# Performance work log

Hardware: AMD Instinct MI355X
Metric: run time of the kernel (lower is better)

## Reference

```python
import jax, jax.numpy as jnp
import numpy as np

B, S, D, H = 8, 1024, 768, 12
DH = D // H
EPS = 1e-5


def setup_inputs() -> dict:
    key = jax.random.key(0)
    ks = jax.random.split(key, 12)
    sc_h = 1.0 / np.sqrt(DH)
    sc_d = 1.0 / np.sqrt(D)
    return {
        "x": jax.random.normal(ks[0], (B, S, D), jnp.float32),
        "ln1_g": jnp.ones((D,), jnp.float32),
        "ln1_b": jnp.zeros((D,), jnp.float32),
        "Wq": jax.random.normal(ks[1], (H, DH, DH), jnp.float32) * sc_h,
        "bq": jax.random.normal(ks[2], (H, DH), jnp.float32) * 0.01,
        "Wk": jax.random.normal(ks[3], (H, DH, DH), jnp.float32) * sc_h,
        "bk": jax.random.normal(ks[4], (H, DH), jnp.float32) * 0.01,
        "Wv": jax.random.normal(ks[5], (H, DH, DH), jnp.float32) * sc_h,
        "bv": jax.random.normal(ks[6], (H, DH), jnp.float32) * 0.01,
        "ln2_g": jnp.ones((D,), jnp.float32),
        "ln2_b": jnp.zeros((D,), jnp.float32),
        "W1": jax.random.normal(ks[7], (D, 4 * D), jnp.float32) * sc_d,  # c_fc (bias=False)
        "W2": jax.random.normal(ks[8], (4 * D, D), jnp.float32) * (1.0 / np.sqrt(4 * D)),  # c_proj (bias=False)
    }


def _layernorm(x, g, b):
    m = jnp.mean(x, axis=-1, keepdims=True)
    v = jnp.mean(jnp.square(x - m), axis=-1, keepdims=True)
    return (x - m) * jax.lax.rsqrt(v + EPS) * g + b


def _msa(x, Wq, bq, Wk, bk, Wv, bv):
    b, s, d = x.shape
    h = x.reshape(b, s, H, DH)  # per-head slices of the embedding
    q = jnp.einsum('bshd,hde->bhse', h, Wq) + bq[None, :, None, :]
    k = jnp.einsum('bshd,hde->bhse', h, Wk) + bk[None, :, None, :]
    v = jnp.einsum('bshd,hde->bhse', h, Wv) + bv[None, :, None, :]
    scores = jnp.einsum('bhse,bhte->bhst', q, k) / np.sqrt(DH).astype(np.float32)
    attn = jax.nn.softmax(scores, axis=-1)
    o = jnp.einsum('bhst,bhte->bhse', attn, v)
    return o.transpose(0, 2, 1, 3).reshape(b, s, d)  # concat heads


def reference(x, ln1_g, ln1_b, Wq, bq, Wk, bk, Wv, bv, ln2_g, ln2_b, W1, W2):
    out = x + _msa(_layernorm(x, ln1_g, ln1_b), Wq, bq, Wk, bk, Wv, bv)
    h = _layernorm(out, ln2_g, ln2_b)
    ffn = jnp.dot(jax.nn.gelu(jnp.dot(h, W1), approximate=False), W2)
    return out + ffn
```

## Files before the change

kernel.cpp:

```cpp
#include <hip/hip_runtime.h>
#include <hip/hip_bf16.h>
#include <math.h>

#define B_ 8
#define S_ 1024
#define D_ 768
#define H_ 12
#define QSCALE 0.18033688011112042f

typedef __attribute__((ext_vector_type(8))) short short8;
typedef __attribute__((ext_vector_type(4))) float floatx4;
typedef unsigned short ushort_t;

__device__ __forceinline__ ushort_t f2bf(float f) {
  unsigned int u = __builtin_bit_cast(unsigned int, f);
  u += 0x7fffu + ((u >> 16) & 1u);
  return (ushort_t)(u >> 16);
}

__device__ __forceinline__ unsigned int pkbf(float a, float b) {
  __hip_bfloat162 h = __float22bfloat162_rn(make_float2(a, b));
  unsigned int r;
  __builtin_memcpy(&r, &h, sizeof(r));
  return r;
}

__device__ __forceinline__ float gelu_f(float x) {
  const float z = fabsf(x) * 0.70710678118654752f;
  const float t = __builtin_amdgcn_rcpf(1.0f + 0.3275911f * z);
  const float p =
      t * (0.254829592f +
           t * (-0.284496736f +
                t * (1.421413741f + t * (-1.453152027f + t * 1.061405429f))));
  const float e = __expf(-z * z);
  const float erfv = 1.0f - p * e;
  return 0.5f * x * (1.0f + copysignf(erfv, x));
}

template <int N>
__device__ __forceinline__ void wait_vmcnt() {
  if constexpr (N == 0)
    asm volatile("s_waitcnt vmcnt(0)" ::: "memory");
  else if constexpr (N == 3)
    asm volatile("s_waitcnt vmcnt(3)" ::: "memory");
  else if constexpr (N == 4)
    asm volatile("s_waitcnt vmcnt(4)" ::: "memory");
  else if constexpr (N == 6)
    asm volatile("s_waitcnt vmcnt(6)" ::: "memory");
  else
    asm volatile("s_waitcnt vmcnt(8)" ::: "memory");
}

__global__ __launch_bounds__(256) void ln_bf16(
    const float* __restrict__ in, const float* __restrict__ g,
    const float* __restrict__ bias, ushort_t* __restrict__ out) {
  const int row = blockIdx.x * 4 + (threadIdx.x >> 6);
  const int lane = threadIdx.x & 63;
  const float* p = in + (size_t)row * D_;
  float4 v[3];
#pragma unroll
  for (int j = 0; j < 3; ++j) v[j] = *(const float4*)(p + j * 256 + lane * 4);
  float s = 0.f;
#pragma unroll
  for (int j = 0; j < 3; ++j) s += (v[j].x + v[j].y) + (v[j].z + v[j].w);
#pragma unroll
  for (int m = 1; m < 64; m <<= 1) s += __shfl_xor(s, m);
  const float mean = s * (1.0f / D_);
  float q = 0.f;
#pragma unroll
  for (int j = 0; j < 3; ++j) {
    const float a = v[j].x - mean, b = v[j].y - mean;
    const float c = v[j].z - mean, d = v[j].w - mean;
    q += (a * a + b * b) + (c * c + d * d);
  }
#pragma unroll
  for (int m = 1; m < 64; m <<= 1) q += __shfl_xor(q, m);
  const float rstd = rsqrtf(q * (1.0f / D_) + 1e-5f);
  ushort_t* o = out + (size_t)row * D_;
#pragma unroll
  for (int j = 0; j < 3; ++j) {
    const float4 gv = *(const float4*)(g + j * 256 + lane * 4);
    const float4 bv = *(const float4*)(bias + j * 256 + lane * 4);
    const unsigned int p01 = pkbf((v[j].x - mean) * rstd * gv.x + bv.x,
                                  (v[j].y - mean) * rstd * gv.y + bv.y);
    const unsigned int p23 = pkbf((v[j].z - mean) * rstd * gv.z + bv.z,
                                  (v[j].w - mean) * rstd * gv.w + bv.w);
    *(uint2*)(o + j * 256 + lane * 4) = make_uint2(p01, p23);
  }
}

__global__ __launch_bounds__(256) void transpose_cast(
    const float* __restrict__ W, ushort_t* __restrict__ Wt, int Kdim, int Ndim) {
  __shared__ float tile[32][33];
  const int n0 = blockIdx.x * 32, k0 = blockIdx.y * 32;
  const int tx = threadIdx.x & 31, ty = threadIdx.x >> 5;
#pragma unroll
  for (int i = 0; i < 32; i += 8)
    tile[ty + i][tx] = W[(size_t)(k0 + ty + i) * Ndim + n0 + tx];
  __syncthreads();
#pragma unroll
  for (int i = 0; i < 32; i += 8)
    Wt[(size_t)(n0 + ty + i) * Kdim + k0 + tx] = f2bf(tile[tx][ty + i]);
}

__global__ __launch_bounds__(256) void trans_w64(
    const float* __restrict__ Wq, const float* __restrict__ Wk,
    const float* __restrict__ Wv, ushort_t* __restrict__ Wqt,
    ushort_t* __restrict__ Wkt, ushort_t* __restrict__ Wvt) {
  const int h = blockIdx.x;
  const float* W = blockIdx.y == 0 ? Wq : blockIdx.y == 1 ? Wk : Wv;
  ushort_t* O = blockIdx.y == 0 ? Wqt : blockIdx.y == 1 ? Wkt : Wvt;
  __shared__ float t[64][65];
  const int tid = threadIdx.x;
#pragma unroll
  for (int i = 0; i < 16; ++i) {
    const int idx = tid + i * 256;
    t[idx >> 6][idx & 63] = W[h * 4096 + idx];
  }
  __syncthreads();
#pragma unroll
  for (int i = 0; i < 16; ++i) {
    const int idx = tid + i * 256;
    O[h * 4096 + idx] = f2bf(t[idx & 63][idx >> 6]);
  }
}

__global__ __launch_bounds__(256) void qkv_mfma(
    const ushort_t* __restrict__ xbf,
    const ushort_t* __restrict__ Wqt, const ushort_t* __restrict__ Wkt,
    const ushort_t* __restrict__ Wvt,
    const float* __restrict__ bq, const float* __restrict__ bk,
    const float* __restrict__ bv,
    ushort_t* __restrict__ qo, ushort_t* __restrict__ ko,
    ushort_t* __restrict__ vt) {
  const int h = blockIdx.y;
  const int mb = blockIdx.x * 128;
  const int tid = threadIdx.x;
  const int wave = tid >> 6, lane = tid & 63;
  const int lc = lane & 15, kq = lane >> 4;
  const int wm = wave * 32;

  __shared__ __align__(16) ushort_t Lb[4][2560];
  ushort_t* Lw = Lb[wave];

  short8 af[2][2];
#pragma unroll
  for (int mi = 0; mi < 2; ++mi)
#pragma unroll
    for (int kc = 0; kc < 2; ++kc)
      af[mi][kc] = *(const short8*)(xbf + (size_t)(mb + wm + mi * 16 + lc) * D_ +
                                    h * 64 + kc * 32 + kq * 8);

  const ushort_t* Wp[3] = {Wqt + h * 4096, Wkt + h * 4096, Wvt + h * 4096};
  floatx4 accT[2][2][4] = {};
  floatx4 accV[2][4] = {};
#pragma unroll
  for (int n = 0; n < 4; ++n)
#pragma unroll
    for (int kc = 0; kc < 2; ++kc) {
      const short8 wq_ = *(const short8*)(Wp[0] + (n * 16 + lc) * 64 +
                                          kc * 32 + kq * 8);
      const short8 wk_ = *(const short8*)(Wp[1] + (n * 16 + lc) * 64 +
                                          kc * 32 + kq * 8);
      const short8 wv_ = *(const short8*)(Wp[2] + (n * 16 + lc) * 64 +
                                          kc * 32 + kq * 8);
#pragma unroll
      for (int mi = 0; mi < 2; ++mi) {
        accT[0][mi][n] = __builtin_amdgcn_mfma_f32_16x16x32_bf16(
            wq_, af[mi][kc], accT[0][mi][n], 0, 0, 0);
        accT[1][mi][n] = __builtin_amdgcn_mfma_f32_16x16x32_bf16(
            wk_, af[mi][kc], accT[1][mi][n], 0, 0, 0);
        accV[mi][n] = __builtin_amdgcn_mfma_f32_16x16x32_bf16(
            af[mi][kc], wv_, accV[mi][n], 0, 0, 0);
      }
    }

  const int b = mb >> 10;
  const size_t obase = (size_t)(b * H_ + h) * (S_ * 64);
  const int sbase = (mb & 1023) + wm;

#pragma unroll
  for (int w3 = 0; w3 < 2; ++w3) {
    const float* bias = (w3 == 0 ? bq : bk) + h * 64;
    ushort_t* outp = w3 == 0 ? qo : ko;
#pragma unroll
    for (int mi = 0; mi < 2; ++mi)
#pragma unroll
      for (int n = 0; n < 4; ++n) {
        const float4 bv4 = *(const float4*)(bias + n * 16 + kq * 4);
        const floatx4 v = accT[w3][mi][n];
        float v0 = v[0] + bv4.x, v1 = v[1] + bv4.y;
        float v2 = v[2] + bv4.z, v3 = v[3] + bv4.w;
        if (w3 == 0) { v0 *= QSCALE; v1 *= QSCALE; v2 *= QSCALE; v3 *= QSCALE; }
        *(uint2*)(&Lw[(mi * 16 + lc) * 72 + n * 16 + kq * 4]) =
            make_uint2(pkbf(v0, v1), pkbf(v2, v3));
      }
    asm volatile("s_waitcnt lgkmcnt(0)" ::: "memory");
    const int srow = lane >> 2, c16 = (lane & 3) * 16;
#pragma unroll
    for (int it = 0; it < 2; ++it) {
      const int s = it * 16 + srow;
      const uint4 r0 = *(const uint4*)(&Lw[s * 72 + c16]);
      const uint4 r1 = *(const uint4*)(&Lw[s * 72 + c16 + 8]);
      *(uint4*)(outp + obase + (size_t)(sbase + s) * 64 + c16) = r0;
      *(uint4*)(outp + obase + (size_t)(sbase + s) * 64 + c16 + 8) = r1;
    }
    asm volatile("s_waitcnt lgkmcnt(0)" ::: "memory");
  }

#pragma unroll
  for (int n = 0; n < 4; ++n) {
    const float bvv = bv[h * 64 + n * 16 + lc];
#pragma unroll
    for (int mi = 0; mi < 2; ++mi) {
      const floatx4 v = accV[mi][n];
      *(uint2*)(&Lw[(n * 16 + lc) * 40 + mi * 16 + kq * 4]) =
          make_uint2(pkbf(v[0] + bvv, v[1] + bvv),
                     pkbf(v[2] + bvv, v[3] + bvv));
    }
  }
  asm volatile("s_waitcnt lgkmcnt(0)" ::: "memory");
  {
    const int erow = lane >> 2, s8 = (lane & 3) * 8;
#pragma unroll
    for (int it = 0; it < 4; ++it) {
      const int e = it * 16 + erow;
      const uint4 r0 = *(const uint4*)(&Lw[e * 40 + s8]);
      *(uint4*)(vt + obase + (size_t)e * S_ + sbase + s8) = r0;
    }
  }
}

__global__ __launch_bounds__(512) void attn_mfma(
    const ushort_t* __restrict__ qb, const ushort_t* __restrict__ kb,
    const ushort_t* __restrict__ vt, const float* __restrict__ x,
    float* __restrict__ out1) {
  const int bh = blockIdx.x;
  const int tid = threadIdx.x;
  const int wave = tid >> 6, lane = tid & 63;
  const int lc = lane & 15, kq = lane >> 4;
  const int q0 = blockIdx.y * 128 + wave * 16;

  __shared__ __align__(16) ushort_t smem[8192 + 8 * 16 * 72];
  ushort_t* Ks = smem;
  ushort_t* Vs = smem + 4096;
  ushort_t* Pp = smem + 8192 + wave * (16 * 72);

  const ushort_t* qp = qb + (size_t)bh * (S_ * 64);
  const ushort_t* kp = kb + (size_t)bh * (S_ * 64);
  const ushort_t* vp = vt + (size_t)bh * (S_ * 64);

  short8 qf[2];
#pragma unroll
  for (int kc = 0; kc < 2; ++kc)
    qf[kc] = *(const short8*)(qp + (size_t)(q0 + lc) * 64 + kc * 32 + kq * 8);

  const int srow = tid >> 3;
  const int sgc = ((tid & 7) ^ (srow & 7)) * 8;
  const int slds = srow * 64 + (tid & 7) * 8;
  const int swz = lc & 7;

  float l_r = 0.0f;
  floatx4 oacc[4] = {};

  for (int kt = 0; kt < 16; ++kt) {
    __builtin_amdgcn_global_load_lds(
        (const __attribute__((address_space(1))) unsigned int*)
            (kp + (size_t)(kt * 64 + srow) * 64 + sgc),
        (__attribute__((address_space(3))) unsigned int*)(Ks + slds), 16, 0, 0);
    __builtin_amdgcn_global_load_lds(
        (const __attribute__((address_space(1))) unsigned int*)
            (vp + (size_t)srow * S_ + kt * 64 + sgc),
        (__attribute__((address_space(3))) unsigned int*)(Vs + slds), 16, 0, 0);
    __syncthreads();

    floatx4 sacc[4] = {};
#pragma unroll
    for (int mi = 0; mi < 4; ++mi) {
      const int row = (mi * 16 + lc) * 64;
#pragma unroll
      for (int kc = 0; kc < 2; ++kc) {
        const short8 kf =
            *(const short8*)(Ks + row + ((kc * 4 + kq) ^ swz) * 8);
        sacc[mi] = __builtin_amdgcn_mfma_f32_16x16x32_bf16(
            kf, qf[kc], sacc[mi], 0, 0, 0);
      }
    }

    float pr[4][4];
    float sm = 0.f;
#pragma unroll
    for (int mi = 0; mi < 4; ++mi)
#pragma unroll
      for (int r = 0; r < 4; ++r) {
        pr[mi][r] = exp2f(sacc[mi][r]);
        sm += pr[mi][r];
      }
    l_r += sm;
#pragma unroll
    for (int mi = 0; mi < 4; ++mi) {
      const unsigned int p01 = pkbf(pr[mi][0], pr[mi][1]);
      const unsigned int p23 = pkbf(pr[mi][2], pr[mi][3]);
      *(uint2*)(&Pp[lc * 72 + mi * 16 + kq * 4]) = make_uint2(p01, p23);
    }
    asm volatile("s_waitcnt lgkmcnt(0)" ::: "memory");

    short8 pf[2];
#pragma unroll
    for (int kc = 0; kc < 2; ++kc)
      pf[kc] = *(const short8*)(&Pp[lc * 72 + kc * 32 + kq * 8]);
#pragma unroll
    for (int mi = 0; mi < 4; ++mi) {
      const int row = (mi * 16 + lc) * 64;
#pragma unroll
      for (int kc = 0; kc < 2; ++kc) {
        const short8 vf =
            *(const short8*)(Vs + row + ((kc * 4 + kq) ^ swz) * 8);
        oacc[mi] = __builtin_amdgcn_mfma_f32_16x16x32_bf16(
            vf, pf[kc], oacc[mi], 0, 0, 0);
      }
    }
    __syncthreads();
  }

  const int b = bh / H_, h = bh % H_;
  float lt = l_r;
  lt += __shfl_xor(lt, 16);
  lt += __shfl_xor(lt, 32);
  const float inv = 1.0f / lt;
  float* Ow = (float*)smem + wave * 1088;
#pragma unroll
  for (int mi = 0; mi < 4; ++mi) {
    floatx4 ov = oacc[mi];
    ov[0] *= inv; ov[1] *= inv; ov[2] *= inv; ov[3] *= inv;
    *(floatx4*)(&Ow[lc * 68 + mi * 16 + kq * 4]) = ov;
  }
  asm volatile("s_waitcnt lgkmcnt(0)" ::: "memory");
  const int row = (lane >> 3) & 7, c8 = (lane & 7) * 4;
#pragma unroll
  for (int rg = 0; rg < 2; ++rg) {
    const int qq = rg * 8 + row;
    const size_t gbase =
        ((size_t)(b * S_) + q0 + qq) * D_ + h * 64 + c8;
#pragma unroll
    for (int j = 0; j < 2; ++j) {
      const float4 ov = *(const float4*)(&Ow[qq * 68 + j * 32 + c8]);
      const float4 xv = *(const float4*)(x + gbase + j * 32);
      *(float4*)(out1 + gbase + j * 32) =
          make_float4(ov.x + xv.x, ov.y + xv.y, ov.z + xv.z, ov.w + xv.w);
    }
  }
}

template <int BM, int BN, int N, int K, bool GELU, bool RESID, bool OUT_BF16,
          bool XCDMAP>
__global__ __launch_bounds__(512, 4) void gemm_pipe(
    const ushort_t* __restrict__ A, const ushort_t* __restrict__ Bt,
    const float* __restrict__ resid, void* __restrict__ Cout) {
  constexpr int MI = BM / 32;
  constexpr int NJ = BN / 64;
  constexpr int LPT = BM / 64 + BN / 64;
  constexpr int NT = K / 64;

  int mb, nb;
  if constexpr (XCDMAP) {
    const int lin = blockIdx.x;
    const int xcd = lin & 7, slot = lin >> 3;
    const int mbg = slot / (N / 128), nbi = slot - mbg * (N / 128);
    mb = (xcd * 16 + mbg) * 64;
    nb = nbi * 128;
  } else {
    nb = blockIdx.x * BN;
    mb = blockIdx.y * BM;
  }

  const int tid = threadIdx.x;
  const int wave = tid >> 6, lane = tid & 63;
  const int wm = (wave >> 2) * (BM / 2), wn = (wave & 3) * (BN / 4);

  __shared__ __align__(16) ushort_t Asp[2][BM * 64];
  __shared__ __align__(16) ushort_t Bsp[2][BN * 64];

  const int sr = tid >> 3;
  const int sc8 = (tid & 7) * 8;
  const int sgx = ((tid & 7) ^ (sr & 7)) * 8;

  auto stage = [&](int t, int buf) {
    const int kb = t * 64;
#pragma unroll
    for (int j = 0; j < BM / 64; ++j) {
      const int row = j * 64 + sr;
      __builtin_amdgcn_global_load_lds(
          (const __attribute__((address_space(1))) unsigned int*)
              (A + (size_t)(mb + row) * K + kb + sgx),
          (__attribute__((address_space(3))) unsigned int*)
              (&Asp[buf][row * 64 + sc8]), 16, 0, 0);
    }
#pragma unroll
    for (int j = 0; j < BN / 64; ++j) {
      const int row = j * 64 + sr;
      __builtin_amdgcn_global_load_lds(
          (const __attribute__((address_space(1))) unsigned int*)
              (Bt + (size_t)(nb + row) * K + kb + sgx),
          (__attribute__((address_space(3))) unsigned int*)
              (&Bsp[buf][row * 64 + sc8]), 16, 0, 0);
    }
  };

  stage(0, 0);
  stage(1, 1);
  wait_vmcnt<LPT>();
  __builtin_amdgcn_s_barrier();
  __builtin_amdgcn_sched_barrier(0);

  const int lc = lane & 15, kq = lane >> 4, swz = lc & 7;
  floatx4 acc[MI][NJ] = {};

#pragma unroll 1
  for (int t = 0; t < NT; ++t) {
    const int cur = t & 1;
    short8 af[MI][2], bfr[NJ][2];
#pragma unroll
    for (int i = 0; i < MI; ++i)
#pragma unroll
      for (int ks = 0; ks < 2; ++ks)
        af[i][ks] = *(const short8*)(&Asp[cur][(wm + i * 16 + lc) * 64 +
                                               ((ks * 4 + kq) ^ swz) * 8]);
#pragma unroll
    for (int j = 0; j < NJ; ++j)
#pragma unroll
      for (int ks = 0; ks < 2; ++ks)
        bfr[j][ks] = *(const short8*)(&Bsp[cur][(wn + j * 16 + lc) * 64 +
                                                ((ks * 4 + kq) ^ swz) * 8]);
    asm volatile("s_waitcnt lgkmcnt(0)" ::: "memory");
    __builtin_amdgcn_sched_barrier(0);
    __builtin_amdgcn_s_barrier();
    __builtin_amdgcn_sched_barrier(0);
    if (t + 2 < NT) stage(t + 2, cur);
    __builtin_amdgcn_sched_barrier(0);
    __builtin_amdgcn_s_setprio(1);
#pragma unroll
    for (int ks = 0; ks < 2; ++ks)
#pragma unroll
      for (int i = 0; i < MI; ++i)
#pragma unroll
        for (int j = 0; j < NJ; ++j)
          acc[i][j] = __builtin_amdgcn_mfma_f32_16x16x32_bf16(
              af[i][ks], bfr[j][ks], acc[i][j], 0, 0, 0);
    __builtin_amdgcn_s_setprio(0);
    if (t + 2 < NT)
      wait_vmcnt<LPT>();
    else if (t + 1 < NT)
      wait_vmcnt<0>();
    if (t + 1 < NT) {
      __builtin_amdgcn_s_barrier();
      __builtin_amdgcn_sched_barrier(0);
    }
  }

  const int lcol = lane & 15, lr4 = (lane >> 4) * 4;
#pragma unroll
  for (int i = 0; i < MI; ++i)
#pragma unroll
    for (int r = 0; r < 4; ++r) {
      const int m = mb + wm + i * 16 + lr4 + r;
#pragma unroll
      for (int j = 0; j < NJ; ++j) {
        const int col = nb + wn + j * 16 + lcol;
        float vv = acc[i][j][r];
        if (GELU) vv = gelu_f(vv);
        if (RESID) vv += resid[(size_t)m * N + col];
        if (OUT_BF16)
          ((ushort_t*)Cout)[(size_t)m * N + col] = f2bf(vv);
        else
          ((float*)Cout)[(size_t)m * N + col] = vv;
      }
    }
}

extern "C" void kernel_launch(void* const* d_in, const int* in_sizes, int n_in,
                              void* d_out, int out_size, void* d_ws, size_t ws_size,
                              hipStream_t stream) {
  (void)in_sizes; (void)n_in; (void)out_size; (void)ws_size;
  const float* x     = (const float*)d_in[0];
  const float* ln1_g = (const float*)d_in[1];
  const float* ln1_b = (const float*)d_in[2];
  const float* Wq    = (const float*)d_in[3];
  const float* bq    = (const float*)d_in[4];
  const float* Wk    = (const float*)d_in[5];
  const float* bk    = (const float*)d_in[6];
  const float* Wv    = (const float*)d_in[7];
  const float* bv    = (const float*)d_in[8];
  const float* ln2_g = (const float*)d_in[9];
  const float* ln2_b = (const float*)d_in[10];
  const float* W1    = (const float*)d_in[11];
  const float* W2    = (const float*)d_in[12];
  float* out = (float*)d_out;

  const size_t n = (size_t)B_ * S_ * D_;
  ushort_t* u = (ushort_t*)d_ws;
  ushort_t* xbf  = u;
  ushort_t* qb   = xbf + n;
  ushort_t* kb   = qb + n;
  ushort_t* vt   = kb + n;
  ushort_t* xbf2 = vt + n;
  ushort_t* act  = xbf2 + n;
  ushort_t* Wt1  = act + (size_t)8192 * 3072;
  ushort_t* Wt2  = Wt1 + (size_t)3072 * 768;
  ushort_t* Wqt  = Wt2 + (size_t)768 * 3072;
  ushort_t* Wkt  = Wqt + H_ * 4096;
  ushort_t* Wvt  = Wkt + H_ * 4096;
  float* out1 = (float*)(Wvt + H_ * 4096);

  trans_w64<<<dim3(12, 3), dim3(256), 0, stream>>>(Wq, Wk, Wv, Wqt, Wkt, Wvt);
  transpose_cast<<<dim3(96, 24), dim3(256), 0, stream>>>(W1, Wt1, 768, 3072);
  transpose_cast<<<dim3(24, 96), dim3(256), 0, stream>>>(W2, Wt2, 3072, 768);
  ln_bf16<<<dim3(2048), dim3(256), 0, stream>>>(x, ln1_g, ln1_b, xbf);
  qkv_mfma<<<dim3(64, 12), dim3(256), 0, stream>>>(xbf, Wqt, Wkt, Wvt,
                                                   bq, bk, bv, qb, kb, vt);
  attn_mfma<<<dim3(96, 8), dim3(512), 0, stream>>>(qb, kb, vt, x, out1);
  ln_bf16<<<dim3(2048), dim3(256), 0, stream>>>(out1, ln2_g, ln2_b, xbf2);
  gemm_pipe<128, 128, 3072, 768, true, false, true, false>
      <<<dim3(24, 64), dim3(512), 0, stream>>>(xbf2, Wt1, nullptr, act);
  gemm_pipe<64, 128, 768, 3072, false, true, false, true>
      <<<dim3(768), dim3(512), 0, stream>>>(act, Wt2, out1, out);
}
```

Measured before the change: 286.1 us.

## Merge weight-prep kernels and split GEMM MFMA around the barrier

```diff
diff --git a/kernel.cpp b/kernel.cpp
--- a/kernel.cpp
+++ b/kernel.cpp
@@ -89,10 +89,11 @@
   }
 }
 
-__global__ __launch_bounds__(256) void transpose_cast(
-    const float* __restrict__ W, ushort_t* __restrict__ Wt, int Kdim, int Ndim) {
-  __shared__ float tile[32][33];
-  const int n0 = blockIdx.x * 32, k0 = blockIdx.y * 32;
+__device__ __forceinline__ void tcast_body(
+    const float* __restrict__ W, ushort_t* __restrict__ Wt,
+    int Kdim, int Ndim, int bx, int by, float* sh) {
+  float(*tile)[33] = (float(*)[33])sh;
+  const int n0 = bx * 32, k0 = by * 32;
   const int tx = threadIdx.x & 31, ty = threadIdx.x >> 5;
 #pragma unroll
   for (int i = 0; i < 32; i += 8)
@@ -103,25 +104,37 @@
     Wt[(size_t)(n0 + ty + i) * Kdim + k0 + tx] = f2bf(tile[tx][ty + i]);
 }
 
-__global__ __launch_bounds__(256) void trans_w64(
+__global__ __launch_bounds__(256) void prep_weights(
+    const float* __restrict__ W1, ushort_t* __restrict__ Wt1,
+    const float* __restrict__ W2, ushort_t* __restrict__ Wt2,
     const float* __restrict__ Wq, const float* __restrict__ Wk,
     const float* __restrict__ Wv, ushort_t* __restrict__ Wqt,
     ushort_t* __restrict__ Wkt, ushort_t* __restrict__ Wvt) {
-  const int h = blockIdx.x;
-  const float* W = blockIdx.y == 0 ? Wq : blockIdx.y == 1 ? Wk : Wv;
-  ushort_t* O = blockIdx.y == 0 ? Wqt : blockIdx.y == 1 ? Wkt : Wvt;
-  __shared__ float t[64][65];
-  const int tid = threadIdx.x;
-#pragma unroll
-  for (int i = 0; i < 16; ++i) {
-    const int idx = tid + i * 256;
-    t[idx >> 6][idx & 63] = W[h * 4096 + idx];
-  }
-  __syncthreads();
-#pragma unroll
-  for (int i = 0; i < 16; ++i) {
-    const int idx = tid + i * 256;
-    O[h * 4096 + idx] = f2bf(t[idx & 63][idx >> 6]);
+  __shared__ float sh[64 * 65];
+  const int bid = blockIdx.x;
+  if (bid < 2304) {
+    tcast_body(W1, Wt1, 768, 3072, bid % 96, bid / 96, sh);
+  } else if (bid < 4608) {
+    const int idx = bid - 2304;
+    tcast_body(W2, Wt2, 3072, 768, idx % 24, idx / 24, sh);
+  } else {
+    const int idx = bid - 4608;
+    const int h = idx % 12, which = idx / 12;
+    const float* W = which == 0 ? Wq : which == 1 ? Wk : Wv;
+    ushort_t* O = which == 0 ? Wqt : which == 1 ? Wkt : Wvt;
+    float(*t)[65] = (float(*)[65])sh;
+    const int tid = threadIdx.x;
+#pragma unroll
+    for (int i = 0; i < 16; ++i) {
+      const int idx2 = tid + i * 256;
+      t[idx2 >> 6][idx2 & 63] = W[h * 4096 + idx2];
+    }
+    __syncthreads();
+#pragma unroll
+    for (int i = 0; i < 16; ++i) {
+      const int idx2 = tid + i * 256;
+      O[h * 4096 + idx2] = f2bf(t[idx2 & 63][idx2 >> 6]);
+    }
   }
 }
 
@@ -421,33 +434,30 @@
     const int cur = t & 1;
     short8 af[MI][2], bfr[NJ][2];
 #pragma unroll
-    for (int i = 0; i < MI; ++i)
-#pragma unroll
-      for (int ks = 0; ks < 2; ++ks)
+    for (int ks = 0; ks < 2; ++ks) {
+#pragma unroll
+      for (int i = 0; i < MI; ++i)
         af[i][ks] = *(const short8*)(&Asp[cur][(wm + i * 16 + lc) * 64 +
                                                ((ks * 4 + kq) ^ swz) * 8]);
 #pragma unroll
-    for (int j = 0; j < NJ; ++j)
-#pragma unroll
-      for (int ks = 0; ks < 2; ++ks)
+      for (int j = 0; j < NJ; ++j)
         bfr[j][ks] = *(const short8*)(&Bsp[cur][(wn + j * 16 + lc) * 64 +
                                                 ((ks * 4 + kq) ^ swz) * 8]);
+    }
+    __builtin_amdgcn_s_setprio(1);
+#pragma unroll
+    for (int i = 0; i < MI; ++i)
+#pragma unroll
+      for (int j = 0; j < NJ; ++j)
+        acc[i][j] = __builtin_amdgcn_mfma_f32_16x16x32_bf16(
+            af[i][0], bfr[j][0], acc[i][j], 0, 0, 0);
+    __builtin_amdgcn_s_setprio(0);
     asm volatile("s_waitcnt lgkmcnt(0)" ::: "memory");
     __builtin_amdgcn_sched_barrier(0);
     __builtin_amdgcn_s_barrier();
     __builtin_amdgcn_sched_barrier(0);
     if (t + 2 < NT) stage(t + 2, cur);
     __builtin_amdgcn_sched_barrier(0);
-    __builtin_amdgcn_s_setprio(1);
-#pragma unroll
-    for (int ks = 0; ks < 2; ++ks)
-#pragma unroll
-      for (int i = 0; i < MI; ++i)
-#pragma unroll
-        for (int j = 0; j < NJ; ++j)
-          acc[i][j] = __builtin_amdgcn_mfma_f32_16x16x32_bf16(
-              af[i][ks], bfr[j][ks], acc[i][j], 0, 0, 0);
-    __builtin_amdgcn_s_setprio(0);
     if (t + 2 < NT)
       wait_vmcnt<LPT>();
     else if (t + 1 < NT)
@@ -456,6 +466,14 @@
       __builtin_amdgcn_s_barrier();
       __builtin_amdgcn_sched_barrier(0);
     }
+    __builtin_amdgcn_s_setprio(1);
+#pragma unroll
+    for (int i = 0; i < MI; ++i)
+#pragma unroll
+      for (int j = 0; j < NJ; ++j)
+        acc[i][j] = __builtin_amdgcn_mfma_f32_16x16x32_bf16(
+            af[i][1], bfr[j][1], acc[i][j], 0, 0, 0);
+    __builtin_amdgcn_s_setprio(0);
   }
 
   const int lcol = lane & 15, lr4 = (lane >> 4) * 4;
@@ -512,9 +530,8 @@
   ushort_t* Wvt  = Wkt + H_ * 4096;
   float* out1 = (float*)(Wvt + H_ * 4096);
 
-  trans_w64<<<dim3(12, 3), dim3(256), 0, stream>>>(Wq, Wk, Wv, Wqt, Wkt, Wvt);
-  transpose_cast<<<dim3(96, 24), dim3(256), 0, stream>>>(W1, Wt1, 768, 3072);
-  transpose_cast<<<dim3(24, 96), dim3(256), 0, stream>>>(W2, Wt2, 3072, 768);
+  prep_weights<<<dim3(4644), dim3(256), 0, stream>>>(
+      W1, Wt1, W2, Wt2, Wq, Wk, Wv, Wqt, Wkt, Wvt);
   ln_bf16<<<dim3(2048), dim3(256), 0, stream>>>(x, ln1_g, ln1_b, xbf);
   qkv_mfma<<<dim3(64, 12), dim3(256), 0, stream>>>(xbf, Wqt, Wkt, Wvt,
                                                    bq, bk, bv, qb, kb, vt);
```

New measurement: 277.7 us. 1.03x faster.
